# Performance work log

Measured on AMD Instinct MI355X. Metric: run time of the kernel, lower is better.

Reference implementation:

```python
import jax, jax.numpy as jnp
import numpy as np

BN_EPS = 1e-5
NORM_EPS = 1e-12  # F.normalize eps
NUM_HEADS = 8
QUERY_DIM = 256
TOP_K = 16


def _l2norm(x):
    n = jnp.linalg.norm(x, axis=-1, keepdims=True)
    return x / jnp.maximum(n, NORM_EPS)


def setup_inputs() -> dict:
    key = jax.random.key(0)
    ks = jax.random.split(key, 8)
    B, S, D, O, N = 2, 512, 1024, 1024, 16384
    return {
        "hidden_states": jax.random.normal(ks[0], (B, S, D), jnp.float32),
        "Wq": jax.random.normal(ks[1], (D, NUM_HEADS * QUERY_DIM), jnp.float32) * 0.02,
        "bq": jnp.zeros((NUM_HEADS * QUERY_DIM,), jnp.float32),
        "bn_gamma": jnp.ones((QUERY_DIM,), jnp.float32),
        "bn_beta": jnp.zeros((QUERY_DIM,), jnp.float32),
        "sub_keys0": jax.random.normal(ks[2], (128, 128), jnp.float32) * 0.02,
        "sub_keys1": jax.random.normal(ks[3], (128, 128), jnp.float32) * 0.02,
        "expert_down": jax.random.normal(ks[4], (N, D), jnp.float32) * 0.02,
        "expert_up": jax.random.normal(ks[5], (N, O), jnp.float32) * 0.02,
    }


def reference(hidden_states, Wq, bq, bn_gamma, bn_beta, sub_keys0, sub_keys1, expert_down, expert_up):
    B, S, D = hidden_states.shape
    H, QD, K = NUM_HEADS, QUERY_DIM, TOP_K

    # query projection -> [B,S,H,QD]
    q = (hidden_states @ Wq + bq).reshape(B, S, H, QD)

    # BatchNorm1d over flattened (B*S*H, QD), training-mode batch stats (biased var)
    qf = q.reshape(-1, QD)
    mean = qf.mean(axis=0)
    var = qf.var(axis=0)
    qf = (qf - mean) * jax.lax.rsqrt(var + BN_EPS) * bn_gamma + bn_beta
    q = qf.reshape(B, S, H, QD)

    # split query into two halves, L2-normalize queries and keys, sub-scores
    half = QD // 2
    s0 = jnp.einsum('bshd,nd->bshn', _l2norm(q[..., :half]), _l2norm(sub_keys0))  # [B,S,H,128]
    s1 = jnp.einsum('bshd,nd->bshn', _l2norm(q[..., half:]), _l2norm(sub_keys1))  # [B,S,H,128]

    # cartesian-product scores: flat expert idx = i*128 + j (matches meshgrid 'ij')
    total = (s0[..., :, None] + s1[..., None, :]).reshape(B, S, H, -1)  # [B,S,H,16384]

    top_scores, top_idx = jax.lax.top_k(total, K)  # [B,S,H,K]
    w = jax.nn.softmax(top_scores, axis=-1)

    dw = expert_down[top_idx]  # [B,S,H,K,D]  (expert_hidden_size = 1)
    uw = expert_up[top_idx]    # [B,S,H,K,O]

    ei = jnp.einsum('bshkd,bsd->bshk', dw, hidden_states)  # per-expert scalar hidden
    eo = jax.nn.gelu(ei, approximate=False)                # F.gelu default = erf
    out = jnp.einsum('bshko,bshk,bshk->bso', uw, eo, w)    # weighted sum over K and H
    return out
```

## Files before the change

kernel.cpp:

```cpp
#include <hip/hip_runtime.h>
#include <math.h>

typedef unsigned long long u64;
typedef unsigned int u32;
typedef unsigned short ushort_t;
typedef _Float16 half8 __attribute__((ext_vector_type(8)));
typedef float f32x4 __attribute__((ext_vector_type(4)));

#define TOKENS 1024
#define DDIM   1024
#define NHEAD  8
#define QD     256
#define HQD    2048
#define NROWS  8192
#define NKEY   128
#define TOPK   16

#define QSCALE 256.0f
#define QINVS  (1.0f / 65536.0f)

__device__ __forceinline__ ushort_t f2bf(float f) {
    u32 u = __float_as_uint(f);
    u32 r = (u + 0x7FFFu + ((u >> 16) & 1u)) >> 16;
    return (ushort_t)r;
}
__device__ __forceinline__ float bf_lo(u32 w) { return __uint_as_float(w << 16); }
__device__ __forceinline__ float bf_hi(u32 w) { return __uint_as_float(w & 0xFFFF0000u); }

__device__ __forceinline__ void hsplit(float x, ushort_t& h, ushort_t& l) {
    _Float16 hh = (_Float16)x;
    float r = x - (float)hh;
    _Float16 ll = (_Float16)r;
    union { _Float16 f; ushort_t u; } c1, c2;
    c1.f = hh; c2.f = ll;
    h = c1.u; l = c2.u;
}

__global__ __launch_bounds__(256) void k_prep1(
    const float* __restrict__ A, const float* __restrict__ W,
    ushort_t* __restrict__ Ab, ushort_t* __restrict__ Wt,
    const float* __restrict__ sk0, const float* __restrict__ sk1,
    float* __restrict__ k0n, float* __restrict__ k1n)
{
    __shared__ __align__(16) char praw[18464];
    const int bid = blockIdx.x;
    const int tid = threadIdx.x;

    if (bid < 128) {
#pragma unroll
        for (int i = 0; i < 8; i++) {
            const int row = bid * 8 + i;
            float4 v = *(const float4*)(A + (size_t)row * 1024 + tid * 4);
            ushort4 h, l;
            hsplit(v.x * QSCALE, h.x, l.x);
            hsplit(v.y * QSCALE, h.y, l.y);
            hsplit(v.z * QSCALE, h.z, l.z);
            hsplit(v.w * QSCALE, h.w, l.w);
            *(ushort4*)(Ab + (size_t)row * 2048 + tid * 4) = h;
            *(ushort4*)(Ab + (size_t)row * 2048 + 1024 + tid * 4) = l;
        }
    } else if (bid < 640) {
        const int cb = bid - 128;
        const int k0 = (cb >> 5) * 64;
        const int n0 = (cb & 31) * 64;
        ushort_t* Lh = (ushort_t*)praw;
        ushort_t* Ll = (ushort_t*)praw + 4608;
        const int nn = (tid & 15) * 4;
        const int kk = tid >> 4;
#pragma unroll
        for (int p = 0; p < 4; p++) {
            const int k = kk + 16 * p;
            float4 v = *(const float4*)(W + (size_t)(k0 + k) * HQD + n0 + nn);
            float xs[4] = {v.x * QSCALE, v.y * QSCALE, v.z * QSCALE, v.w * QSCALE};
#pragma unroll
            for (int j = 0; j < 4; j++) {
                ushort_t h, l;
                hsplit(xs[j], h, l);
                Lh[(nn + j) * 72 + k] = h;
                Ll[(nn + j) * 72 + k] = l;
            }
        }
        __syncthreads();
#pragma unroll
        for (int e = 0; e < 2; e++) {
            const int idx = tid + 256 * e;
            const int n = idx >> 3, ks = idx & 7;
            uint4 hv = *(const uint4*)(Lh + n * 72 + ks * 8);
            uint4 lv = *(const uint4*)(Ll + n * 72 + ks * 8);
            *(uint4*)(Wt + (size_t)(n0 + n) * 2048 + k0 + ks * 8) = hv;
            *(uint4*)(Wt + (size_t)(n0 + n) * 2048 + 1024 + k0 + ks * 8) = lv;
        }
    } else {
        float* fs = (float*)praw;
        const int b2 = bid - 640;
        const int sub = tid >> 7;
        const int col = tid & 127;
        const int gr = b2 * 2 + sub;
        const float* src = (gr < 128) ? sk0 : sk1;
        float* dst = (gr < 128) ? k0n : k1n;
        const int row = gr & 127;
        float v = src[row * 128 + col];
        float sq = v * v;
        for (int off = 32; off; off >>= 1) sq += __shfl_down(sq, off);
        if ((tid & 63) == 0) fs[tid >> 6] = sq;
        __syncthreads();
        if ((tid & 127) == 0) {
            float n = sqrtf(fs[tid >> 6] + fs[(tid >> 6) + 1]);
            fs[8 + sub] = 1.0f / fmaxf(n, 1e-12f);
        }
        __syncthreads();
        dst[row * 128 + col] = v * fs[8 + sub];
    }
}

__global__ __launch_bounds__(256) void k_fused2(
    const ushort_t* __restrict__ Ab, const ushort_t* __restrict__ Wt,
    float* __restrict__ qp,
    const float* __restrict__ down, const float* __restrict__ up,
    ushort_t* __restrict__ downb, ushort_t* __restrict__ upb)
{
    __shared__ __align__(16) char lds[2][16384];
    const int tid = threadIdx.x;
    const int bid = blockIdx.x;

    if (bid >= 512) {
        const int cb = bid - 512;
        const float* src = (cb < 1024) ? down : up;
        ushort_t* dst = (cb < 1024) ? downb : upb;
        const size_t base4 = (size_t)(cb & 1023) * 4096;
        const float4* s4 = (const float4*)src;
        ushort4* d4 = (ushort4*)dst;
#pragma unroll 4
        for (int it = 0; it < 16; it++) {
            size_t i = base4 + (size_t)it * 256 + tid;
            float4 v = s4[i];
            ushort4 o;
            o.x = f2bf(v.x); o.y = f2bf(v.y); o.z = f2bf(v.z); o.w = f2bf(v.w);
            d4[i] = o;
        }
        return;
    }

    const int m0 = (bid >> 5) * 64;
    const int n0 = (bid & 31) * 64;

    const int srow = tid >> 2;
    const int scol = (tid & 3) * 16;
    const int swz = (srow & 7) << 4;

    const int lane = tid & 63;
    const int w = tid >> 6;
    const int wmb = (w >> 1) * 32;
    const int wnb = (w & 1) * 32;
    const int fr = lane & 15;
    const int kg = lane >> 4;
    const int rswz = (fr & 7) << 4;

    f32x4 acc[2][2];
#pragma unroll
    for (int i = 0; i < 2; i++)
#pragma unroll
        for (int j = 0; j < 2; j++)
            acc[i][j] = (f32x4){0.f, 0.f, 0.f, 0.f};

    uint4 ar0, ar1, br0, br1;

    auto LOADR = [&](int gs) {
        const int term = gs >> 4;
        const int aoff = (term == 1) ? 1024 : 0;
        const int woff = (term == 2) ? 1024 : 0;
        const int kb = (gs & 15) * 64;
        const ushort_t* ap = Ab + (size_t)(m0 + srow) * 2048 + aoff + kb + scol;
        const ushort_t* wp = Wt + (size_t)(n0 + srow) * 2048 + woff + kb + scol;
        ar0 = *(const uint4*)(ap);
        ar1 = *(const uint4*)(ap + 8);
        br0 = *(const uint4*)(wp);
        br1 = *(const uint4*)(wp + 8);
    };
    auto WLDS = [&](int buf) {
        char* As = lds[buf];
        char* Bs = lds[buf] + 8192;
        const int b0 = (srow * 128 + scol * 2) ^ swz;
        const int b1 = (srow * 128 + scol * 2 + 16) ^ swz;
        *(uint4*)(As + b0) = ar0;
        *(uint4*)(As + b1) = ar1;
        *(uint4*)(Bs + b0) = br0;
        *(uint4*)(Bs + b1) = br1;
    };

    LOADR(0);
    WLDS(0);

    for (int s = 0; s < 48; s++) {
        __syncthreads();
        if (s < 47) LOADR(s + 1);
        const char* As = lds[s & 1];
        const char* Bs = lds[s & 1] + 8192;
#pragma unroll
        for (int kh = 0; kh < 2; kh++) {
            half8 a[2], b[2];
#pragma unroll
            for (int f = 0; f < 2; f++) {
                const int rowA = wmb + f * 16 + fr;
                a[f] = *(const half8*)(As + ((rowA * 128 + kh * 64 + kg * 16) ^ rswz));
                const int rowB = wnb + f * 16 + fr;
                b[f] = *(const half8*)(Bs + ((rowB * 128 + kh * 64 + kg * 16) ^ rswz));
            }
#pragma unroll
            for (int fm = 0; fm < 2; fm++)
#pragma unroll
                for (int fn = 0; fn < 2; fn++)
                    acc[fm][fn] = __builtin_amdgcn_mfma_f32_16x16x32_f16(
                        a[fm], b[fn], acc[fm][fn], 0, 0, 0);
        }
        if (s < 47) WLDS((s + 1) & 1);
    }

#pragma unroll
    for (int fm = 0; fm < 2; fm++) {
        const int rbase = m0 + wmb + fm * 16 + kg * 4;
#pragma unroll
        for (int fn = 0; fn < 2; fn++) {
            const int c = n0 + wnb + fn * 16 + fr;
#pragma unroll
            for (int j = 0; j < 4; j++)
                qp[(size_t)(rbase + j) * HQD + c] = acc[fm][fn][j];
        }
    }
}

__global__ __launch_bounds__(256) void k_bnstat1(const float* __restrict__ qp,
                                                 const float* __restrict__ bq,
                                                 float* __restrict__ psum,
                                                 float* __restrict__ psq,
                                                 float qsc)
{
    const int b = blockIdx.x;
    const int j = threadIdx.x;
    float s = 0.f, sq = 0.f;
#pragma unroll 4
    for (int rr = 0; rr < 16; rr++) {
        const int r = b * 16 + rr;
        const size_t g = (size_t)r * 256 + j;
        float v = qp[g] * qsc + bq[(r & 7) * 256 + j];
        s += v; sq += v * v;
    }
    psum[b * 256 + j] = s;
    psq[b * 256 + j]  = sq;
}

__global__ __launch_bounds__(256) void k_bnstat2(const float* __restrict__ psum,
                                                 const float* __restrict__ psq,
                                                 const float* __restrict__ gamma,
                                                 float* __restrict__ meanOut,
                                                 float* __restrict__ scaleOut)
{
    const int j = threadIdx.x;
    float s = 0.f, sq = 0.f;
    for (int b = 0; b < 512; b++) {
        s += psum[b * 256 + j];
        sq += psq[b * 256 + j];
    }
    float mean = s * (1.0f / 8192.0f);
    float var = sq * (1.0f / 8192.0f) - mean * mean;
    meanOut[j] = mean;
    scaleOut[j] = gamma[j] / sqrtf(var + 1e-5f);
}

__global__ __launch_bounds__(256) void k_scores(const float* __restrict__ qp,
                                                const float* __restrict__ bq,
                                                const float* __restrict__ mean,
                                                const float* __restrict__ scale,
                                                const float* __restrict__ beta,
                                                const float* __restrict__ kn0,
                                                const float* __restrict__ kn1,
                                                float* __restrict__ sOut0,
                                                float* __restrict__ sOut1,
                                                float qsc)
{
    __shared__ float Qs[128 * 68];
    __shared__ float Ks[64 * 132];
    __shared__ float rp[4][64];
    __shared__ float invn[64];
    const int half = blockIdx.y;
    const int row0 = blockIdx.x * 64;
    const int tid = threadIdx.x;

    {
        const int d4 = (tid & 31) * 4;
        const int rbase = tid >> 5;
        const int j4 = half * 128 + d4;
        float4 m4 = *(const float4*)(mean + j4);
        float4 sc4 = *(const float4*)(scale + j4);
        float4 be4 = *(const float4*)(beta + j4);
        float4 bi4 = *(const float4*)(bq + rbase * 256 + j4);
#pragma unroll
        for (int p = 0; p < 8; p++) {
            const int rr = rbase + p * 8;
            const int row = row0 + rr;
            const size_t g = (size_t)(row >> 3) * 2048 + (size_t)rbase * 256 + j4;
            float4 a = *(const float4*)(qp + g);
            float x0 = (a.x * qsc + bi4.x - m4.x) * sc4.x + be4.x;
            float x1 = (a.y * qsc + bi4.y - m4.y) * sc4.y + be4.y;
            float x2 = (a.z * qsc + bi4.z - m4.z) * sc4.z + be4.z;
            float x3 = (a.w * qsc + bi4.w - m4.w) * sc4.w + be4.w;
            Qs[(d4 + 0) * 68 + rr] = x0;
            Qs[(d4 + 1) * 68 + rr] = x1;
            Qs[(d4 + 2) * 68 + rr] = x2;
            Qs[(d4 + 3) * 68 + rr] = x3;
        }
    }
    __syncthreads();
    {
        const int r = tid & 63, qd = tid >> 6;
        float s = 0.f;
#pragma unroll 8
        for (int d = qd * 32; d < qd * 32 + 32; d++) {
            float v = Qs[d * 68 + r];
            s += v * v;
        }
        rp[qd][r] = s;
    }
    __syncthreads();
    if (tid < 64) {
        float s = rp[0][tid] + rp[1][tid] + rp[2][tid] + rp[3][tid];
        invn[tid] = 1.0f / fmaxf(sqrtf(s), 1e-12f);
    }

    const float* kn = half ? kn1 : kn0;
    float* sOut = half ? sOut1 : sOut0;
    const int ty = tid >> 5;
    const int tx = tid & 31;
    float acc[8][4] = {};

    for (int c = 0; c < 2; c++) {
        __syncthreads();
        {
            int dd4 = (tid & 15) * 4;
            int n = tid >> 4;
#pragma unroll
            for (int p = 0; p < 8; p++) {
                int nn = n + p * 16;
                float4 v = *(const float4*)(kn + nn * 128 + c * 64 + dd4);
                Ks[(dd4 + 0) * 132 + nn] = v.x; Ks[(dd4 + 1) * 132 + nn] = v.y;
                Ks[(dd4 + 2) * 132 + nn] = v.z; Ks[(dd4 + 3) * 132 + nn] = v.w;
            }
        }
        __syncthreads();
#pragma unroll
        for (int d = 0; d < 64; d++) {
            float a[8], b[4];
            *(float4*)(a)     = *(const float4*)&Qs[(c * 64 + d) * 68 + ty * 8];
            *(float4*)(a + 4) = *(const float4*)&Qs[(c * 64 + d) * 68 + ty * 8 + 4];
            *(float4*)(b)     = *(const float4*)&Ks[d * 132 + tx * 4];
#pragma unroll
            for (int i = 0; i < 8; i++)
#pragma unroll
                for (int j = 0; j < 4; j++)
                    acc[i][j] = fmaf(a[i], b[j], acc[i][j]);
        }
    }
#pragma unroll
    for (int i = 0; i < 8; i++) {
        const float iv = invn[ty * 8 + i];
        float4 r;
        r.x = acc[i][0] * iv; r.y = acc[i][1] * iv;
        r.z = acc[i][2] * iv; r.w = acc[i][3] * iv;
        *(float4*)(sOut + (size_t)(row0 + ty * 8 + i) * 128 + tx * 4) = r;
    }
}

__device__ __forceinline__ u64 mkkey(float v, u32 idx) {
    u32 ub = __float_as_uint(v);
    ub = (ub & 0x80000000u) ? ~ub : (ub | 0x80000000u);
    return ((u64)ub << 32) | (u64)(0xFFFFFFFFu - idx);
}
__device__ __forceinline__ float keyval(u64 k) {
    u32 ub = (u32)(k >> 32);
    u32 fb = (ub & 0x80000000u) ? (ub ^ 0x80000000u) : ~ub;
    return __uint_as_float(fb);
}
__device__ __forceinline__ u32 keyidx(u64 k) {
    return 0xFFFFFFFFu - (u32)(k & 0xFFFFFFFFu);
}

__global__ __launch_bounds__(256) void k_topk(const float* __restrict__ s0,
                                              const float* __restrict__ s1,
                                              int* __restrict__ tIdx,
                                              float* __restrict__ tW)
{
    __shared__ float shv[4][2][16];
    __shared__ int   shi[4][2][16];
    const int w = threadIdx.x >> 6;
    const int lane = threadIdx.x & 63;
    const int row = blockIdx.x * 4 + w;

#pragma unroll
    for (int h = 0; h < 2; h++) {
        const float* s = h ? s1 : s0;
        float v0 = s[(size_t)row * 128 + lane];
        float v1 = s[(size_t)row * 128 + 64 + lane];
        u64 k0 = mkkey(v0, (u32)lane);
        u64 k1 = mkkey(v1, (u32)(lane + 64));
        for (int r = 0; r < 16; r++) {
            u64 m = (k0 > k1) ? k0 : k1;
#pragma unroll
            for (int off = 1; off < 64; off <<= 1) {
                u64 o = __shfl_xor(m, off);
                if (o > m) m = o;
            }
            if (k0 == m) k0 = 0;
            if (k1 == m) k1 = 0;
            if (lane == 0) { shv[w][h][r] = keyval(m); shi[w][h][r] = (int)keyidx(m); }
        }
    }

    u64 ck[4];
#pragma unroll
    for (int qq = 0; qq < 4; qq++) {
        int id = lane + 64 * qq;
        int a = id >> 4, b = id & 15;
        float v = shv[w][0][a] + shv[w][1][b];
        u32 idx = (u32)(shi[w][0][a] * 128 + shi[w][1][b]);
        ck[qq] = mkkey(v, idx);
    }
    float winv = 0.f; u32 wini = 0;
    for (int r = 0; r < 16; r++) {
        u64 m = ck[0];
#pragma unroll
        for (int qq = 1; qq < 4; qq++) if (ck[qq] > m) m = ck[qq];
#pragma unroll
        for (int off = 1; off < 64; off <<= 1) {
            u64 o = __shfl_xor(m, off);
            if (o > m) m = o;
        }
#pragma unroll
        for (int qq = 0; qq < 4; qq++) if (ck[qq] == m) ck[qq] = 0;
        if (lane == r) { winv = keyval(m); wini = keyidx(m); }
    }
    float vmax = __shfl(winv, 0);
    if (lane < 16) {
        float e = expf(winv - vmax);
        float ssum = e;
#pragma unroll
        for (int off = 1; off < 16; off <<= 1) ssum += __shfl_xor(ssum, off, 16);
        tW[(size_t)row * 16 + lane] = e / ssum;
        tIdx[(size_t)row * 16 + lane] = (int)wini;
    }
}

__global__ __launch_bounds__(1024) void k_coef_bf(const float* __restrict__ hidden,
                                                  const ushort_t* __restrict__ downb,
                                                  const int* __restrict__ tIdx,
                                                  const float* __restrict__ tW,
                                                  float* __restrict__ coef)
{
    const int t = blockIdx.x;
    const int wave = threadIdx.x >> 6, lane = threadIdx.x & 63;
    const float* hp = hidden + (size_t)t * 1024;
    float h[16];
    *(float4*)(h + 0)  = *(const float4*)(hp + lane * 8);
    *(float4*)(h + 4)  = *(const float4*)(hp + lane * 8 + 4);
    *(float4*)(h + 8)  = *(const float4*)(hp + 512 + lane * 8);
    *(float4*)(h + 12) = *(const float4*)(hp + 512 + lane * 8 + 4);

#pragma unroll
    for (int g = 0; g < 2; g++) {
        const int pg = wave * 8 + g * 4;
        float s[4];
        uint4 a[4], b[4];
#pragma unroll
        for (int i = 0; i < 4; i++) {
            const int e = tIdx[(size_t)t * 128 + pg + i];
            const uint4* rp = (const uint4*)(downb + (size_t)e * 1024);
            a[i] = rp[lane];
            b[i] = rp[lane + 64];
        }
#pragma unroll
        for (int i = 0; i < 4; i++) {
            float acc = 0.f;
            const u32* aw = (const u32*)&a[i];
            const u32* bw = (const u32*)&b[i];
#pragma unroll
            for (int c = 0; c < 4; c++) {
                acc = fmaf(bf_lo(aw[c]), h[2 * c], acc);
                acc = fmaf(bf_hi(aw[c]), h[2 * c + 1], acc);
                acc = fmaf(bf_lo(bw[c]), h[8 + 2 * c], acc);
                acc = fmaf(bf_hi(bw[c]), h[8 + 2 * c + 1], acc);
            }
            s[i] = acc;
        }
#pragma unroll
        for (int i = 0; i < 4; i++)
#pragma unroll
            for (int off = 1; off < 64; off <<= 1) s[i] += __shfl_xor(s[i], off);
        if (lane < 4) {
            float x = (lane == 0) ? s[0] : (lane == 1) ? s[1] : (lane == 2) ? s[2] : s[3];
            float wv = tW[(size_t)t * 128 + pg + lane];
            float gl = 0.5f * x * (1.0f + erff(x * 0.70710678118654752f));
            coef[(size_t)t * 128 + pg + lane] = wv * gl;
        }
    }
}

__global__ __launch_bounds__(1024) void k_coef_f32(const float* __restrict__ hidden,
                                                   const float* __restrict__ down,
                                                   const int* __restrict__ tIdx,
                                                   const float* __restrict__ tW,
                                                   float* __restrict__ coef)
{
    __shared__ __align__(16) float hs[1024];
    __shared__ int   eidx[128];
    __shared__ float wv[128];
    const int t = blockIdx.x;
    const int tid = threadIdx.x;
    hs[tid] = hidden[(size_t)t * 1024 + tid];
    if (tid < 128) {
        eidx[tid] = tIdx[(size_t)t * 128 + tid];
        wv[tid]   = tW[(size_t)t * 128 + tid];
    }
    __syncthreads();
    const int wave = tid >> 6, lane = tid & 63;
#pragma unroll 2
    for (int i = 0; i < 8; i++) {
        const int p = wave * 8 + i;
        const float4* dp = (const float4*)(down + (size_t)eidx[p] * 1024);
        float sum = 0.f;
#pragma unroll
        for (int c = 0; c < 4; c++) {
            float4 dv = dp[lane + 64 * c];
            float4 hv = *(const float4*)(hs + (lane + 64 * c) * 4);
            sum += dv.x * hv.x + dv.y * hv.y + dv.z * hv.z + dv.w * hv.w;
        }
        for (int off = 32; off; off >>= 1) sum += __shfl_down(sum, off);
        if (lane == 0) {
            float x = sum;
            float g = 0.5f * x * (1.0f + erff(x * 0.70710678118654752f));
            coef[(size_t)t * 128 + p] = wv[p] * g;
        }
    }
}

__global__ __launch_bounds__(256) void k_accum_bf(const ushort_t* __restrict__ upb,
                                                  const int* __restrict__ tIdx,
                                                  const float* __restrict__ coef,
                                                  float* __restrict__ out)
{
    __shared__ float cf[128];
    __shared__ int   ei[128];
    __shared__ float part[512];
    const int t = blockIdx.x >> 1;
    const int jh = blockIdx.x & 1;
    const int tid = threadIdx.x;
    if (tid < 128) {
        cf[tid] = coef[(size_t)t * 128 + tid];
        ei[tid] = tIdx[(size_t)t * 128 + tid];
    }
    __syncthreads();
    const int half = tid >> 7;
    const int jl = (tid & 127) * 4;
    const int j4 = jh * 512 + jl;
    float acc[4] = {};
    const int p0 = half * 64;
#pragma unroll 16
    for (int p = p0; p < p0 + 64; p++) {
        const float c = cf[p];
        uint2 v = *(const uint2*)(upb + (size_t)ei[p] * 1024 + j4);
        acc[0] = fmaf(c, bf_lo(v.x), acc[0]);
        acc[1] = fmaf(c, bf_hi(v.x), acc[1]);
        acc[2] = fmaf(c, bf_lo(v.y), acc[2]);
        acc[3] = fmaf(c, bf_hi(v.y), acc[3]);
    }
    if (half == 0) *(float4*)&part[jl] = *(float4*)acc;
    __syncthreads();
    if (half == 1) {
        float4 pv = *(float4*)&part[jl];
        float4 r;
        r.x = acc[0] + pv.x; r.y = acc[1] + pv.y;
        r.z = acc[2] + pv.z; r.w = acc[3] + pv.w;
        *(float4*)(out + (size_t)t * 1024 + j4) = r;
    }
}

__global__ __launch_bounds__(256) void k_accum_f32(const float* __restrict__ up,
                                                   const int* __restrict__ tIdx,
                                                   const float* __restrict__ coef,
                                                   float* __restrict__ out)
{
    __shared__ float cf[128];
    __shared__ int   ei[128];
    const int t = blockIdx.x >> 2;
    const int c = blockIdx.x & 3;
    const int tid = threadIdx.x;
    if (tid < 128) {
        cf[tid] = coef[(size_t)t * 128 + tid];
        ei[tid] = tIdx[(size_t)t * 128 + tid];
    }
    __syncthreads();
    const int j = c * 256 + tid;
    float acc = 0.f;
#pragma unroll 8
    for (int p = 0; p < 128; p++)
        acc = fmaf(cf[p], up[(size_t)ei[p] * 1024 + j], acc);
    out[(size_t)t * 1024 + j] = acc;
}

__global__ __launch_bounds__(256) void k_fall1(
    const float* __restrict__ A, const float* __restrict__ W,
    float* __restrict__ qp,
    const float* __restrict__ sk0, const float* __restrict__ sk1,
    float* __restrict__ k0n, float* __restrict__ k1n)
{
    __shared__ float smem[2 * 32 * 68];
    const int bid = blockIdx.x;
    const int tid = threadIdx.x;

    if (bid < 512) {
        float* As = smem;
        float* Bs = smem + 32 * 68;
        const int m0 = (bid >> 5) * 64;
        const int n0 = (bid & 31) * 64;
        const int aM  = tid >> 3;
        const int aK4 = (tid & 7) * 4;
        const int bK  = tid >> 4;
        const int bN4 = (tid & 15) * 4;
        const int ty  = tid >> 4;
        const int tx  = tid & 15;
        float acc[4][4] = {};
        for (int kk = 0; kk < 1024; kk += 32) {
            __syncthreads();
#pragma unroll
            for (int p = 0; p < 2; p++) {
                int m = aM + 32 * p;
                float4 v = *(const float4*)(A + (size_t)(m0 + m) * DDIM + kk + aK4);
                As[(aK4 + 0) * 68 + m] = v.x; As[(aK4 + 1) * 68 + m] = v.y;
                As[(aK4 + 2) * 68 + m] = v.z; As[(aK4 + 3) * 68 + m] = v.w;
            }
#pragma unroll
            for (int p = 0; p < 2; p++) {
                int k = bK + 16 * p;
                float4 v = *(const float4*)(W + (size_t)(kk + k) * HQD + n0 + bN4);
                *(float4*)&Bs[k * 68 + bN4] = v;
            }
            __syncthreads();
#pragma unroll
            for (int k = 0; k < 32; k++) {
                float a[4], b[4];
                *(float4*)(a) = *(const float4*)&As[k * 68 + ty * 4];
                *(float4*)(b) = *(const float4*)&Bs[k * 68 + tx * 4];
#pragma unroll
                for (int i = 0; i < 4; i++)
#pragma unroll
                    for (int j = 0; j < 4; j++)
                        acc[i][j] = fmaf(a[i], b[j], acc[i][j]);
            }
        }
#pragma unroll
        for (int i = 0; i < 4; i++) {
            int m = m0 + ty * 4 + i;
            float4 r;
            r.x = acc[i][0]; r.y = acc[i][1]; r.z = acc[i][2]; r.w = acc[i][3];
            *(float4*)(qp + (size_t)m * HQD + n0 + tx * 4) = r;
        }
    } else {
        const int b2 = bid - 512;
        const int sub = tid >> 7;
        const int col = tid & 127;
        const int gr = b2 * 2 + sub;
        const float* src = (gr < 128) ? sk0 : sk1;
        float* dst = (gr < 128) ? k0n : k1n;
        const int row = gr & 127;
        float v = src[row * 128 + col];
        float sq = v * v;
        for (int off = 32; off; off >>= 1) sq += __shfl_down(sq, off);
        if ((tid & 63) == 0) smem[tid >> 6] = sq;
        __syncthreads();
        if ((tid & 127) == 0) {
            float n = sqrtf(smem[tid >> 6] + smem[(tid >> 6) + 1]);
            smem[8 + sub] = 1.0f / fmaxf(n, 1e-12f);
        }
        __syncthreads();
        dst[row * 128 + col] = v * smem[8 + sub];
    }
}

extern "C" void kernel_launch(void* const* d_in, const int* in_sizes, int n_in,
                              void* d_out, int out_size, void* d_ws, size_t ws_size,
                              hipStream_t stream)
{
    const float* hidden = (const float*)d_in[0];
    const float* Wq     = (const float*)d_in[1];
    const float* bq     = (const float*)d_in[2];
    const float* gamma  = (const float*)d_in[3];
    const float* beta   = (const float*)d_in[4];
    const float* sk0    = (const float*)d_in[5];
    const float* sk1    = (const float*)d_in[6];
    const float* down   = (const float*)d_in[7];
    const float* up     = (const float*)d_in[8];
    float* out = (float*)d_out;

    float* ws = (float*)d_ws;
    size_t o = 0;
    float* qp    = ws + o; o += (size_t)TOKENS * HQD;
    float* ps    = ws + o; o += 512 * 256;
    float* pq    = ws + o; o += 512 * 256;
    float* meanb = ws + o; o += 256;
    float* scaleb= ws + o; o += 256;
    float* k0n   = ws + o; o += NKEY * 128;
    float* k1n   = ws + o; o += NKEY * 128;
    float* s0    = ws + o; o += (size_t)NROWS * 128;
    float* s1    = ws + o; o += (size_t)NROWS * 128;
    float* tW    = ws + o; o += (size_t)NROWS * TOPK;
    int*   tIdx  = (int*)(ws + o); o += (size_t)NROWS * TOPK;
    float* coef  = ws + o; o += (size_t)TOKENS * 128;
    ushort_t* downb = (ushort_t*)(ws + o); o += (size_t)16384 * 1024 / 2;
    ushort_t* upb   = (ushort_t*)(ws + o); o += (size_t)16384 * 1024 / 2;
    ushort_t* Ab    = (ushort_t*)(ws + o); o += (size_t)1024 * 2048 / 2;
    ushort_t* Wt    = (ushort_t*)(ws + o); o += (size_t)2048 * 2048 / 2;
    const int useBF = (ws_size >= o * sizeof(float)) ? 1 : 0;
    const float qsc = useBF ? QINVS : 1.0f;

    if (useBF) {
        k_prep1 <<<768, 256, 0, stream>>>(hidden, Wq, Ab, Wt, sk0, sk1, k0n, k1n);
        k_fused2<<<2560, 256, 0, stream>>>(Ab, Wt, qp, down, up, downb, upb);
    } else {
        k_fall1 <<<640, 256, 0, stream>>>(hidden, Wq, qp, sk0, sk1, k0n, k1n);
    }
    k_bnstat1<<<512, 256, 0, stream>>>(qp, bq, ps, pq, qsc);
    k_bnstat2<<<1, 256, 0, stream>>>(ps, pq, gamma, meanb, scaleb);
    k_scores <<<dim3(128, 2), 256, 0, stream>>>(qp, bq, meanb, scaleb, beta,
                                                k0n, k1n, s0, s1, qsc);
    k_topk   <<<2048, 256, 0, stream>>>(s0, s1, tIdx, tW);
    if (useBF) {
        k_coef_bf <<<TOKENS, 1024, 0, stream>>>(hidden, downb, tIdx, tW, coef);
        k_accum_bf<<<2048, 256, 0, stream>>>(upb, tIdx, coef, out);
    } else {
        k_coef_f32 <<<TOKENS, 1024, 0, stream>>>(hidden, down, tIdx, tW, coef);
        k_accum_f32<<<4096, 256, 0, stream>>>(up, tIdx, coef, out);
    }
}
```

Before: 225.2 us.

## Spread expert weight bf16 conversion across later kernels to overlap with small stages

The fp32-to-bf16 conversion of expert_down and expert_up used to run entirely as extra blocks of the projection GEMM kernel. It is now split into chunks handled by extra blocks appended to the GEMM, bnstat1, scores, topk and coef kernels. Every chunk is still converted before the kernel that reads it. The aim is to fill idle GPU capacity in the small, latency-bound stages with bandwidth-bound conversion work. The cost is that the conversion blocks may slow the critical-path blocks of those kernels, and k_scores changes from a 2D to a flattened 1D grid.

```diff
diff --git a/kernel.cpp b/kernel.cpp
--- a/kernel.cpp
+++ b/kernel.cpp
@@ -34,6 +34,27 @@
     union { _Float16 f; ushort_t u; } c1, c2;
     c1.f = hh; c2.f = ll;
     h = c1.u; l = c2.u;
+}
+
+template<int NTHR, int ITERS>
+__device__ __forceinline__ void cvt_chunk(int gcb, int tid,
+                                          const float* __restrict__ down,
+                                          const float* __restrict__ up,
+                                          ushort_t* __restrict__ downb,
+                                          ushort_t* __restrict__ upb) {
+    const float* src = (gcb < 1024) ? down : up;
+    ushort_t* dst = (gcb < 1024) ? downb : upb;
+    const size_t base4 = (size_t)(gcb & 1023) * 4096;
+    const float4* s4 = (const float4*)src;
+    ushort4* d4 = (ushort4*)dst;
+#pragma unroll 4
+    for (int it = 0; it < ITERS; it++) {
+        size_t i = base4 + (size_t)it * NTHR + tid;
+        float4 v = s4[i];
+        ushort4 o;
+        o.x = f2bf(v.x); o.y = f2bf(v.y); o.z = f2bf(v.z); o.w = f2bf(v.w);
+        d4[i] = o;
+    }
 }
 
 __global__ __launch_bounds__(256) void k_prep1(
@@ -124,20 +145,7 @@
     const int bid = blockIdx.x;
 
     if (bid >= 512) {
-        const int cb = bid - 512;
-        const float* src = (cb < 1024) ? down : up;
-        ushort_t* dst = (cb < 1024) ? downb : upb;
-        const size_t base4 = (size_t)(cb & 1023) * 4096;
-        const float4* s4 = (const float4*)src;
-        ushort4* d4 = (ushort4*)dst;
-#pragma unroll 4
-        for (int it = 0; it < 16; it++) {
-            size_t i = base4 + (size_t)it * 256 + tid;
-            float4 v = s4[i];
-            ushort4 o;
-            o.x = f2bf(v.x); o.y = f2bf(v.y); o.z = f2bf(v.z); o.w = f2bf(v.w);
-            d4[i] = o;
-        }
+        cvt_chunk<256, 16>(bid - 512, tid, down, up, downb, upb);
         return;
     }
 
@@ -233,10 +241,18 @@
                                                  const float* __restrict__ bq,
                                                  float* __restrict__ psum,
                                                  float* __restrict__ psq,
-                                                 float qsc)
+                                                 float qsc,
+                                                 const float* __restrict__ down,
+                                                 const float* __restrict__ up,
+                                                 ushort_t* __restrict__ downb,
+                                                 ushort_t* __restrict__ upb)
 {
     const int b = blockIdx.x;
     const int j = threadIdx.x;
+    if (b >= 512) {
+        cvt_chunk<256, 16>(512 + (b - 512), j, down, up, downb, upb);
+        return;
+    }
     float s = 0.f, sq = 0.f;
 #pragma unroll 4
     for (int rr = 0; rr < 16; rr++) {
@@ -276,15 +292,24 @@
                                                 const float* __restrict__ kn1,
                                                 float* __restrict__ sOut0,
                                                 float* __restrict__ sOut1,
-                                                float qsc)
+                                                float qsc,
+                                                const float* __restrict__ down,
+                                                const float* __restrict__ up,
+                                                ushort_t* __restrict__ downb,
+                                                ushort_t* __restrict__ upb)
 {
     __shared__ float Qs[128 * 68];
     __shared__ float Ks[64 * 132];
     __shared__ float rp[4][64];
     __shared__ float invn[64];
-    const int half = blockIdx.y;
-    const int row0 = blockIdx.x * 64;
+    const int bid = blockIdx.x;
     const int tid = threadIdx.x;
+    if (bid >= 256) {
+        cvt_chunk<256, 16>(768 + (bid - 256), tid, down, up, downb, upb);
+        return;
+    }
+    const int half = bid >> 7;
+    const int row0 = (bid & 127) * 64;
 
     {
         const int d4 = (tid & 31) * 4;
@@ -387,13 +412,22 @@
 __global__ __launch_bounds__(256) void k_topk(const float* __restrict__ s0,
                                               const float* __restrict__ s1,
                                               int* __restrict__ tIdx,
-                                              float* __restrict__ tW)
+                                              float* __restrict__ tW,
+                                              const float* __restrict__ down,
+                                              const float* __restrict__ up,
+                                              ushort_t* __restrict__ downb,
+                                              ushort_t* __restrict__ upb)
 {
     __shared__ float shv[4][2][16];
     __shared__ int   shi[4][2][16];
+    const int bid = blockIdx.x;
+    if (bid >= 2048) {
+        cvt_chunk<256, 16>(1024 + (bid - 2048), threadIdx.x, down, up, downb, upb);
+        return;
+    }
     const int w = threadIdx.x >> 6;
     const int lane = threadIdx.x & 63;
-    const int row = blockIdx.x * 4 + w;
+    const int row = bid * 4 + w;
 
 #pragma unroll
     for (int h = 0; h < 2; h++) {
@@ -453,9 +487,17 @@
                                                   const ushort_t* __restrict__ downb,
                                                   const int* __restrict__ tIdx,
                                                   const float* __restrict__ tW,
-                                                  float* __restrict__ coef)
+                                                  float* __restrict__ coef,
+                                                  const float* __restrict__ down,
+                                                  const float* __restrict__ up,
+                                                  ushort_t* __restrict__ downb2,
+                                                  ushort_t* __restrict__ upb)
 {
     const int t = blockIdx.x;
+    if (t >= 1024) {
+        cvt_chunk<1024, 4>(1536 + (t - 1024), threadIdx.x, down, up, downb2, upb);
+        return;
+    }
     const int wave = threadIdx.x >> 6, lane = threadIdx.x & 63;
     const float* hp = hidden + (size_t)t * 1024;
     float h[16];
@@ -722,19 +764,24 @@
 
     if (useBF) {
         k_prep1 <<<768, 256, 0, stream>>>(hidden, Wq, Ab, Wt, sk0, sk1, k0n, k1n);
-        k_fused2<<<2560, 256, 0, stream>>>(Ab, Wt, qp, down, up, downb, upb);
+        k_fused2<<<1024, 256, 0, stream>>>(Ab, Wt, qp, down, up, downb, upb);
+        k_bnstat1<<<768, 256, 0, stream>>>(qp, bq, ps, pq, qsc, down, up, downb, upb);
+        k_bnstat2<<<1, 256, 0, stream>>>(ps, pq, gamma, meanb, scaleb);
+        k_scores <<<512, 256, 0, stream>>>(qp, bq, meanb, scaleb, beta,
+                                           k0n, k1n, s0, s1, qsc,
+                                           down, up, downb, upb);
+        k_topk   <<<2560, 256, 0, stream>>>(s0, s1, tIdx, tW, down, up, downb, upb);
+        k_coef_bf<<<1536, 1024, 0, stream>>>(hidden, downb, tIdx, tW, coef,
+                                             down, up, downb, upb);
+        k_accum_bf<<<2048, 256, 0, stream>>>(upb, tIdx, coef, out);
     } else {
         k_fall1 <<<640, 256, 0, stream>>>(hidden, Wq, qp, sk0, sk1, k0n, k1n);
-    }
-    k_bnstat1<<<512, 256, 0, stream>>>(qp, bq, ps, pq, qsc);
-    k_bnstat2<<<1, 256, 0, stream>>>(ps, pq, gamma, meanb, scaleb);
-    k_scores <<<dim3(128, 2), 256, 0, stream>>>(qp, bq, meanb, scaleb, beta,
-                                                k0n, k1n, s0, s1, qsc);
-    k_topk   <<<2048, 256, 0, stream>>>(s0, s1, tIdx, tW);
-    if (useBF) {
-        k_coef_bf <<<TOKENS, 1024, 0, stream>>>(hidden, downb, tIdx, tW, coef);
-        k_accum_bf<<<2048, 256, 0, stream>>>(upb, tIdx, coef, out);
-    } else {
+        k_bnstat1<<<512, 256, 0, stream>>>(qp, bq, ps, pq, qsc, down, up, downb, upb);
+        k_bnstat2<<<1, 256, 0, stream>>>(ps, pq, gamma, meanb, scaleb);
+        k_scores <<<256, 256, 0, stream>>>(qp, bq, meanb, scaleb, beta,
+                                           k0n, k1n, s0, s1, qsc,
+                                           down, up, downb, upb);
+        k_topk   <<<2048, 256, 0, stream>>>(s0, s1, tIdx, tW, down, up, downb, upb);
         k_coef_f32 <<<TOKENS, 1024, 0, stream>>>(hidden, down, tIdx, tW, coef);
         k_accum_f32<<<4096, 256, 0, stream>>>(up, tIdx, coef, out);
     }
```

After: 222.1 us. No clear change (-1.4%).
